# Optimization experiments

Measured on AMD Instinct MI355X. Metric: run time of the kernel, lower is better.

## Reference

```python
import jax, jax.numpy as jnp
import numpy as np
from jax import lax

B, T, D = 8, 2048, 1024


def setup_inputs() -> dict:
    key = jax.random.key(0)
    ks = jax.random.split(key, 8)
    s = 1.0 / np.sqrt(D)
    x = jax.random.normal(ks[0], (B, T, D), dtype=jnp.float32)
    Wq = jax.random.uniform(ks[1], (D, D), jnp.float32, -s, s)
    bq = jax.random.uniform(ks[2], (D,), jnp.float32, -s, s)
    Wk = jax.random.uniform(ks[3], (D, D), jnp.float32, -s, s)
    bk = jax.random.uniform(ks[4], (D,), jnp.float32, -s, s)
    Wv = jax.random.uniform(ks[5], (D, D), jnp.float32, -s, s)
    bv = jax.random.uniform(ks[6], (D,), jnp.float32, -s, s)
    decay = jnp.full((D,), 0.9, dtype=jnp.float32)  # nn.Parameter(ones*0.9)
    return {"x": x, "Wq": Wq, "bq": bq, "Wk": Wk, "bk": bk,
            "Wv": Wv, "bv": bv, "decay": decay}


def reference(x, Wq, bq, Wk, bk, Wv, bv, decay):
    # projections (torch Linear: x @ W.T + b)
    q = jnp.einsum('btd,ed->bte', x, Wq) + bq
    k = jnp.einsum('btd,ed->bte', x, Wk) + bk
    v = jnp.einsum('btd,ed->bte', x, Wv) + bv
    kv = k * v  # [B,T,D]

    # diagonal-decay linear recurrence: mem_t = decay * mem_{t-1} + kv_t
    def step(mem, kv_t):
        mem = decay * mem + kv_t  # [B,D]
        return mem, mem

    mem0 = jnp.zeros((B, D), dtype=x.dtype)
    _, mems = lax.scan(step, mem0, jnp.swapaxes(kv, 0, 1))  # mems: [T,B,D]
    out = q * jnp.swapaxes(mems, 0, 1)  # output_t = q_t * mem_t
    return out
```

## Files before the change

### kernel.cpp

```cpp
#include <hip/hip_runtime.h>
#include <cstdint>

typedef unsigned short ushort_t;
typedef __bf16 bf16x8 __attribute__((ext_vector_type(8)));
typedef float f32x4 __attribute__((ext_vector_type(4)));

#define B_ 8
#define T_ 2048
#define D_ 1024
#define M_ (B_ * T_)
#define NCHUNK 64
#define CHUNKLEN 32

__device__ __forceinline__ ushort_t f2bf(float f) {
    union { float f; uint32_t u; } v; v.f = f;
    uint32_t u = v.u;
    uint32_t r = (u + 0x7fffu + ((u >> 16) & 1u)) >> 16;
    return (ushort_t)r;
}
__device__ __forceinline__ float bf2f(ushort_t h) {
    union { uint32_t u; float f; } v; v.u = ((uint32_t)h) << 16;
    return v.f;
}

__device__ __forceinline__ void async16(const ushort_t* g, ushort_t* l) {
    __builtin_amdgcn_global_load_lds(
        (const __attribute__((address_space(1))) void*)g,
        (__attribute__((address_space(3))) void*)l, 16, 0, 0);
}

__global__ __launch_bounds__(256) void cast_all(
    const float* __restrict__ x, const float* __restrict__ wq,
    const float* __restrict__ wk, const float* __restrict__ wv,
    ushort_t* __restrict__ xb, ushort_t* __restrict__ Wb) {
    const int nx4 = M_ * D_ / 4, nw4 = D_ * D_ / 4;
    int i = blockIdx.x * blockDim.x + threadIdx.x;
    const float* src; ushort_t* dstp; int si;
    if (i < nx4) {
        src = x; si = i; dstp = xb + (size_t)i * 4;
    } else {
        int j = i - nx4;
        dstp = Wb + (size_t)j * 4;
        if (j < nw4)          { src = wq; si = j; }
        else if (j < 2 * nw4) { src = wk; si = j - nw4; }
        else                  { src = wv; si = j - 2 * nw4; }
    }
    float4 v = ((const float4*)src)[si];
    ushort4 o;
    o.x = f2bf(v.x); o.y = f2bf(v.y); o.z = f2bf(v.z); o.w = f2bf(v.w);
    *(ushort4*)dstp = o;
}

__global__ __launch_bounds__(256, 2) void gemm_qkv(
    const ushort_t* __restrict__ xb, const ushort_t* __restrict__ Wq,
    const ushort_t* __restrict__ Wk, const ushort_t* __restrict__ Wv,
    const float* __restrict__ bq, const float* __restrict__ bk,
    const float* __restrict__ bv,
    ushort_t* __restrict__ qb, ushort_t* __restrict__ kvb) {
    __shared__ ushort_t As[128 * 32];
    __shared__ ushort_t B0[128 * 32];
    __shared__ ushort_t B1[128 * 32];

    const int idx = blockIdx.x;
    const bool qmode = idx < 512;
    int mb, n0;
    const ushort_t *W0, *W1;
    if (qmode) {
        mb = idx & 127; n0 = (idx >> 7) * 256;
        W0 = Wq + (size_t)n0 * D_;
        W1 = Wq + (size_t)(n0 + 128) * D_;
    } else {
        const int j = idx - 512;
        mb = j & 127; n0 = (j >> 7) * 128;
        W0 = Wk + (size_t)n0 * D_;
        W1 = Wv + (size_t)n0 * D_;
    }
    const int m0 = mb * 128;

    const int t = threadIdx.x;
    const int lane = t & 63, wv = t >> 6;
    const int wr = (wv >> 1) * 64, wc = (wv & 1) * 64;

    f32x4 acc0[4][4], acc1[4][4];
#pragma unroll
    for (int i = 0; i < 4; ++i)
#pragma unroll
        for (int j = 0; j < 4; ++j) {
            acc0[i][j] = (f32x4){0.f, 0.f, 0.f, 0.f};
            acc1[i][j] = (f32x4){0.f, 0.f, 0.f, 0.f};
        }

    const int r0 = t >> 2, r1 = r0 + 64;
    const int sc = ((t & 3) ^ ((r0 >> 1) & 3)) * 8;

    const int swq = ((lane & 15) >> 1) & 3;
    const int csel = (((lane >> 4) ^ swq)) * 8;
    const int rowa = wr + (lane & 15);
    const int rowb = wc + (lane & 15);

    for (int kt = 0; kt < 32; ++kt) {
        const int k0 = kt * 32;
        async16(xb + (size_t)(m0 + r0) * D_ + k0 + sc, &As[t * 8]);
        async16(xb + (size_t)(m0 + r1) * D_ + k0 + sc, &As[(t + 256) * 8]);
        async16(W0 + (size_t)r0 * D_ + k0 + sc, &B0[t * 8]);
        async16(W0 + (size_t)r1 * D_ + k0 + sc, &B0[(t + 256) * 8]);
        async16(W1 + (size_t)r0 * D_ + k0 + sc, &B1[t * 8]);
        async16(W1 + (size_t)r1 * D_ + k0 + sc, &B1[(t + 256) * 8]);
        __syncthreads();

        bf16x8 af[4], b08[4], b18[4];
#pragma unroll
        for (int i = 0; i < 4; ++i)
            af[i] = *(const bf16x8*)&As[(rowa + i * 16) * 32 + csel];
#pragma unroll
        for (int j = 0; j < 4; ++j) {
            b08[j] = *(const bf16x8*)&B0[(rowb + j * 16) * 32 + csel];
            b18[j] = *(const bf16x8*)&B1[(rowb + j * 16) * 32 + csel];
        }
#pragma unroll
        for (int i = 0; i < 4; ++i)
#pragma unroll
            for (int j = 0; j < 4; ++j) {
                acc0[i][j] = __builtin_amdgcn_mfma_f32_16x16x32_bf16(
                    af[i], b08[j], acc0[i][j], 0, 0, 0);
                acc1[i][j] = __builtin_amdgcn_mfma_f32_16x16x32_bf16(
                    af[i], b18[j], acc1[i][j], 0, 0, 0);
            }
        __syncthreads();
    }

    const float* bias0 = qmode ? (bq + n0) : (bk + n0);
    const float* bias1 = qmode ? (bq + n0 + 128) : (bv + n0);
    const int colq = lane & 15;
    const int rowq = (lane >> 4) * 4;
#pragma unroll
    for (int i = 0; i < 4; ++i) {
#pragma unroll
        for (int j = 0; j < 4; ++j) {
            const int c = wc + j * 16 + colq;
            const float bv0 = bias0[c], bv1 = bias1[c];
#pragma unroll
            for (int r = 0; r < 4; ++r) {
                const int rg = m0 + wr + i * 16 + rowq + r;
                if (qmode) {
                    qb[(size_t)rg * D_ + n0 + c]       = f2bf(acc0[i][j][r] + bv0);
                    qb[(size_t)rg * D_ + n0 + 128 + c] = f2bf(acc1[i][j][r] + bv1);
                } else {
                    const float kf = acc0[i][j][r] + bv0;
                    const float vf = acc1[i][j][r] + bv1;
                    kvb[(size_t)rg * D_ + n0 + c] = f2bf(kf * vf);
                }
            }
        }
    }
}

__global__ __launch_bounds__(256) void scan_chunks(
    const ushort_t* __restrict__ kvb, const float* __restrict__ decay,
    float* __restrict__ S) {
    const int b = blockIdx.x >> 6;
    const int c = blockIdx.x & 63;
    const int d0 = threadIdx.x * 4;
    const float4 dc = *(const float4*)&decay[d0];
    float m0 = 0.f, m1 = 0.f, m2 = 0.f, m3 = 0.f;
    size_t base = ((size_t)b * T_ + c * CHUNKLEN) * D_ + d0;
#pragma unroll 8
    for (int i = 0; i < CHUNKLEN; ++i) {
        ushort4 kv = *(const ushort4*)&kvb[base + (size_t)i * D_];
        m0 = fmaf(dc.x, m0, bf2f(kv.x));
        m1 = fmaf(dc.y, m1, bf2f(kv.y));
        m2 = fmaf(dc.z, m2, bf2f(kv.z));
        m3 = fmaf(dc.w, m3, bf2f(kv.w));
    }
    *(float4*)&S[((size_t)b * NCHUNK + c) * D_ + d0] = make_float4(m0, m1, m2, m3);
}

__global__ __launch_bounds__(256) void scan_carry(
    const float* __restrict__ S, const float* __restrict__ decay,
    float* __restrict__ P) {
    const int idx = blockIdx.x * blockDim.x + threadIdx.x;
    const int d = idx & (D_ - 1), b = idx >> 10;
    const float dec = decay[d];
    float dL = dec;
    dL *= dL; dL *= dL; dL *= dL; dL *= dL; dL *= dL;
    float p = 0.f;
    for (int c = 0; c < NCHUNK; ++c) {
        const size_t o = ((size_t)b * NCHUNK + c) * D_ + d;
        P[o] = p;
        p = fmaf(dL, p, S[o]);
    }
}

__global__ __launch_bounds__(256) void scan_final(
    const ushort_t* __restrict__ kvb, const ushort_t* __restrict__ qb,
    const float* __restrict__ decay, const float* __restrict__ P,
    float* __restrict__ out) {
    const int b = blockIdx.x >> 6;
    const int c = blockIdx.x & 63;
    const int d0 = threadIdx.x * 4;
    const float4 dc = *(const float4*)&decay[d0];
    const float4 p4 = *(const float4*)&P[((size_t)b * NCHUNK + c) * D_ + d0];
    float m0 = p4.x, m1 = p4.y, m2 = p4.z, m3 = p4.w;
    size_t base = ((size_t)b * T_ + c * CHUNKLEN) * D_ + d0;
#pragma unroll 8
    for (int i = 0; i < CHUNKLEN; ++i) {
        const size_t o = base + (size_t)i * D_;
        ushort4 kv = *(const ushort4*)&kvb[o];
        ushort4 q4 = *(const ushort4*)&qb[o];
        m0 = fmaf(dc.x, m0, bf2f(kv.x));
        m1 = fmaf(dc.y, m1, bf2f(kv.y));
        m2 = fmaf(dc.z, m2, bf2f(kv.z));
        m3 = fmaf(dc.w, m3, bf2f(kv.w));
        *(float4*)&out[o] = make_float4(bf2f(q4.x) * m0, bf2f(q4.y) * m1,
                                        bf2f(q4.z) * m2, bf2f(q4.w) * m3);
    }
}

extern "C" void kernel_launch(void* const* d_in, const int* in_sizes, int n_in,
                              void* d_out, int out_size, void* d_ws, size_t ws_size,
                              hipStream_t stream) {
    const float* x     = (const float*)d_in[0];
    const float* Wq    = (const float*)d_in[1];
    const float* bq    = (const float*)d_in[2];
    const float* Wk    = (const float*)d_in[3];
    const float* bk    = (const float*)d_in[4];
    const float* Wv    = (const float*)d_in[5];
    const float* bv    = (const float*)d_in[6];
    const float* decay = (const float*)d_in[7];
    float* out = (float*)d_out;

    char* ws = (char*)d_ws;
    ushort_t* xb  = (ushort_t*)(ws);
    ushort_t* Wb  = (ushort_t*)(ws + 33554432);
    ushort_t* qb  = (ushort_t*)(ws + 39845888);
    ushort_t* kvb = (ushort_t*)(ws + 73400320);
    float*    S   = (float*)(ws);
    float*    P   = (float*)(ws + 2097152);

    ushort_t* Wqb = Wb;
    ushort_t* Wkb = Wb + D_ * D_;
    ushort_t* Wvb = Wb + 2 * D_ * D_;

    const int ncast = (M_ * D_ / 4) + (3 * D_ * D_ / 4);
    cast_all<<<ncast / 256, 256, 0, stream>>>(x, Wq, Wk, Wv, xb, Wb);

    gemm_qkv<<<1536, 256, 0, stream>>>(xb, Wqb, Wkb, Wvb, bq, bk, bv, qb, kvb);

    scan_chunks<<<B_ * NCHUNK, 256, 0, stream>>>(kvb, decay, S);
    scan_carry<<<(B_ * D_) / 256, 256, 0, stream>>>(S, decay, P);
    scan_final<<<B_ * NCHUNK, 256, 0, stream>>>(kvb, qb, decay, P, out);
}
```

Measured before the change: 279.2 us.

## Fuse chunk-sum scan into GEMM epilogue and fold carry into final scan

The k*v GEMM epilogue now computes decay-weighted per-chunk partial sums directly from accumulator registers, using cross-lane shuffles, and writes the chunk summaries S. This removes the scan_chunks re-read of kvb. The separate scan_carry kernel is dropped; each scan_final2 block instead recomputes its own prefix carry by looping over all earlier chunk summaries. That trades two launches and one kvb pass for redundant carry work that grows with chunk index, plus extra epilogue arithmetic in the GEMM.

```diff
diff --git a/kernel.cpp b/kernel.cpp
--- a/kernel.cpp
+++ b/kernel.cpp
@@ -55,8 +55,9 @@
     const ushort_t* __restrict__ xb, const ushort_t* __restrict__ Wq,
     const ushort_t* __restrict__ Wk, const ushort_t* __restrict__ Wv,
     const float* __restrict__ bq, const float* __restrict__ bk,
-    const float* __restrict__ bv,
-    ushort_t* __restrict__ qb, ushort_t* __restrict__ kvb) {
+    const float* __restrict__ bv, const float* __restrict__ decay,
+    ushort_t* __restrict__ qb, ushort_t* __restrict__ kvb,
+    float* __restrict__ S) {
     __shared__ ushort_t As[128 * 32];
     __shared__ ushort_t B0[128 * 32];
     __shared__ ushort_t B1[128 * 32];
@@ -129,78 +130,102 @@
         __syncthreads();
     }
 
-    const float* bias0 = qmode ? (bq + n0) : (bk + n0);
-    const float* bias1 = qmode ? (bq + n0 + 128) : (bv + n0);
     const int colq = lane & 15;
-    const int rowq = (lane >> 4) * 4;
-#pragma unroll
-    for (int i = 0; i < 4; ++i) {
+    const int quad = lane >> 4;
+    const int rowq = quad * 4;
+
+    if (qmode) {
+        const float* bias0 = bq + n0;
+        const float* bias1 = bq + n0 + 128;
+#pragma unroll
+        for (int i = 0; i < 4; ++i) {
+#pragma unroll
+            for (int j = 0; j < 4; ++j) {
+                const int c = wc + j * 16 + colq;
+                const float bv0 = bias0[c], bv1 = bias1[c];
+#pragma unroll
+                for (int r = 0; r < 4; ++r) {
+                    const int rg = m0 + wr + i * 16 + rowq + r;
+                    qb[(size_t)rg * D_ + n0 + c]       = f2bf(acc0[i][j][r] + bv0);
+                    qb[(size_t)rg * D_ + n0 + 128 + c] = f2bf(acc1[i][j][r] + bv1);
+                }
+            }
+        }
+    } else {
+        const float* bias0 = bk + n0;
+        const float* bias1 = bv + n0;
+        const int bidx = m0 >> 11;
+        const int cbase = ((m0 & 2047) >> 5) + (wr >> 5);
+        float s0[4], s1[4];
+#pragma unroll
+        for (int j = 0; j < 4; ++j) { s0[j] = 0.f; s1[j] = 0.f; }
+
 #pragma unroll
         for (int j = 0; j < 4; ++j) {
             const int c = wc + j * 16 + colq;
             const float bv0 = bias0[c], bv1 = bias1[c];
-#pragma unroll
-            for (int r = 0; r < 4; ++r) {
-                const int rg = m0 + wr + i * 16 + rowq + r;
-                if (qmode) {
-                    qb[(size_t)rg * D_ + n0 + c]       = f2bf(acc0[i][j][r] + bv0);
-                    qb[(size_t)rg * D_ + n0 + 128 + c] = f2bf(acc1[i][j][r] + bv1);
-                } else {
+            const float dec = decay[n0 + c];
+            const float d2 = dec * dec, d4 = d2 * d2;
+            const float d8 = d4 * d4, d16 = d8 * d8;
+            const float d3 = d2 * dec;
+            const float d4p3 = d8 * d4;
+            const float P1 = (quad == 0) ? d4p3 : ((quad == 1) ? d8 : ((quad == 2) ? d4 : 1.0f));
+            const float P0 = d16 * P1;
+            const float wr3[4] = {d3, d2, dec, 1.0f};
+#pragma unroll
+            for (int i = 0; i < 4; ++i) {
+                const float base_w = (i & 1) ? P1 : P0;
+#pragma unroll
+                for (int r = 0; r < 4; ++r) {
+                    const int rg = m0 + wr + i * 16 + rowq + r;
                     const float kf = acc0[i][j][r] + bv0;
                     const float vf = acc1[i][j][r] + bv1;
-                    kvb[(size_t)rg * D_ + n0 + c] = f2bf(kf * vf);
+                    const float kvf = kf * vf;
+                    kvb[(size_t)rg * D_ + n0 + c] = f2bf(kvf);
+                    const float wgt = base_w * wr3[r];
+                    if (i < 2) s0[j] = fmaf(kvf, wgt, s0[j]);
+                    else       s1[j] = fmaf(kvf, wgt, s1[j]);
                 }
             }
         }
-    }
-}
-
-__global__ __launch_bounds__(256) void scan_chunks(
-    const ushort_t* __restrict__ kvb, const float* __restrict__ decay,
-    float* __restrict__ S) {
-    const int b = blockIdx.x >> 6;
-    const int c = blockIdx.x & 63;
-    const int d0 = threadIdx.x * 4;
-    const float4 dc = *(const float4*)&decay[d0];
-    float m0 = 0.f, m1 = 0.f, m2 = 0.f, m3 = 0.f;
-    size_t base = ((size_t)b * T_ + c * CHUNKLEN) * D_ + d0;
-#pragma unroll 8
-    for (int i = 0; i < CHUNKLEN; ++i) {
-        ushort4 kv = *(const ushort4*)&kvb[base + (size_t)i * D_];
-        m0 = fmaf(dc.x, m0, bf2f(kv.x));
-        m1 = fmaf(dc.y, m1, bf2f(kv.y));
-        m2 = fmaf(dc.z, m2, bf2f(kv.z));
-        m3 = fmaf(dc.w, m3, bf2f(kv.w));
-    }
-    *(float4*)&S[((size_t)b * NCHUNK + c) * D_ + d0] = make_float4(m0, m1, m2, m3);
-}
-
-__global__ __launch_bounds__(256) void scan_carry(
-    const float* __restrict__ S, const float* __restrict__ decay,
-    float* __restrict__ P) {
-    const int idx = blockIdx.x * blockDim.x + threadIdx.x;
-    const int d = idx & (D_ - 1), b = idx >> 10;
-    const float dec = decay[d];
-    float dL = dec;
-    dL *= dL; dL *= dL; dL *= dL; dL *= dL; dL *= dL;
-    float p = 0.f;
-    for (int c = 0; c < NCHUNK; ++c) {
-        const size_t o = ((size_t)b * NCHUNK + c) * D_ + d;
-        P[o] = p;
-        p = fmaf(dL, p, S[o]);
-    }
-}
-
-__global__ __launch_bounds__(256) void scan_final(
+#pragma unroll
+        for (int j = 0; j < 4; ++j) {
+            s0[j] += __shfl_xor(s0[j], 16, 64);
+            s0[j] += __shfl_xor(s0[j], 32, 64);
+            s1[j] += __shfl_xor(s1[j], 16, 64);
+            s1[j] += __shfl_xor(s1[j], 32, 64);
+        }
+        if (quad == 0) {
+#pragma unroll
+            for (int j = 0; j < 4; ++j) {
+                const int cg = n0 + wc + j * 16 + colq;
+                S[(((size_t)bidx * NCHUNK) + cbase) * D_ + cg]     = s0[j];
+                S[(((size_t)bidx * NCHUNK) + cbase + 1) * D_ + cg] = s1[j];
+            }
+        }
+    }
+}
+
+__global__ __launch_bounds__(256) void scan_final2(
     const ushort_t* __restrict__ kvb, const ushort_t* __restrict__ qb,
-    const float* __restrict__ decay, const float* __restrict__ P,
+    const float* __restrict__ decay, const float* __restrict__ S,
     float* __restrict__ out) {
     const int b = blockIdx.x >> 6;
     const int c = blockIdx.x & 63;
     const int d0 = threadIdx.x * 4;
     const float4 dc = *(const float4*)&decay[d0];
-    const float4 p4 = *(const float4*)&P[((size_t)b * NCHUNK + c) * D_ + d0];
-    float m0 = p4.x, m1 = p4.y, m2 = p4.z, m3 = p4.w;
+    float e0 = dc.x, e1 = dc.y, e2 = dc.z, e3 = dc.w;
+#pragma unroll
+    for (int s = 0; s < 5; ++s) { e0 *= e0; e1 *= e1; e2 *= e2; e3 *= e3; }
+    float m0 = 0.f, m1 = 0.f, m2 = 0.f, m3 = 0.f;
+    const float* Sb = &S[((size_t)b * NCHUNK) * D_ + d0];
+    for (int cc = 0; cc < c; ++cc) {
+        float4 s4 = *(const float4*)&Sb[(size_t)cc * D_];
+        m0 = fmaf(e0, m0, s4.x);
+        m1 = fmaf(e1, m1, s4.y);
+        m2 = fmaf(e2, m2, s4.z);
+        m3 = fmaf(e3, m3, s4.w);
+    }
     size_t base = ((size_t)b * T_ + c * CHUNKLEN) * D_ + d0;
 #pragma unroll 8
     for (int i = 0; i < CHUNKLEN; ++i) {
@@ -234,8 +259,7 @@
     ushort_t* Wb  = (ushort_t*)(ws + 33554432);
     ushort_t* qb  = (ushort_t*)(ws + 39845888);
     ushort_t* kvb = (ushort_t*)(ws + 73400320);
-    float*    S   = (float*)(ws);
-    float*    P   = (float*)(ws + 2097152);
+    float*    S   = (float*)(ws + 106954752);
 
     ushort_t* Wqb = Wb;
     ushort_t* Wkb = Wb + D_ * D_;
@@ -244,9 +268,8 @@
     const int ncast = (M_ * D_ / 4) + (3 * D_ * D_ / 4);
     cast_all<<<ncast / 256, 256, 0, stream>>>(x, Wq, Wk, Wv, xb, Wb);
 
-    gemm_qkv<<<1536, 256, 0, stream>>>(xb, Wqb, Wkb, Wvb, bq, bk, bv, qb, kvb);
-
-    scan_chunks<<<B_ * NCHUNK, 256, 0, stream>>>(kvb, decay, S);
-    scan_carry<<<(B_ * D_) / 256, 256, 0, stream>>>(S, decay, P);
-    scan_final<<<B_ * NCHUNK, 256, 0, stream>>>(kvb, qb, decay, P, out);
-}
+    gemm_qkv<<<1536, 256, 0, stream>>>(xb, Wqb, Wkb, Wvb, bq, bk, bv, decay,
+                                       qb, kvb, S);
+
+    scan_final2<<<B_ * NCHUNK, 256, 0, stream>>>(kvb, qb, decay, S, out);
+}
```

New measurement: 272.7 us. 2.3% less time.
